# Optimization experiments

Measured on AMD Instinct MI355X. Metric: run time of the kernel, lower is better.

The kernel has to match this reference:

```python
import jax, jax.numpy as jnp
import numpy as np

NUM_GRAPHS = 1024
NODES_PER_GRAPH = 128
NUM_EDGES = 1048576
D_IN = 128          # n_heads * head_out_feats = input/concat dim
ATT_HEADS = 2       # intra/inter GATConv(d, 32, 2) as in HDN-DDI repo
ATT_OUT = 32
POOL_HEADS = 2      # pool = GATConv(128, 64, 2)
POOL_OUT = 64
EPS = 1e-5          # PyG LayerNorm eps


def _segment_softmax(e, seg, n):
    # numerically-stable softmax over edges grouped by destination node
    m = jax.ops.segment_max(e, seg, num_segments=n)
    m = jnp.where(jnp.isfinite(m), m, 0.0)
    p = jnp.exp(e - m[seg])
    s = jax.ops.segment_sum(p, seg, num_segments=n)
    return p / (s[seg] + 1e-16)


def _gat(x_src, x_dst, edge_index, w_src, w_dst, att_src, att_dst, bias, self_loops):
    # PyG GATConv: linear -> per-head attention logits -> leaky_relu(0.2) ->
    # softmax over incoming edges -> weighted sum of source features -> concat heads + bias
    H, C = att_src.shape
    nd = x_dst.shape[0]
    hs = (x_src @ w_src).reshape(-1, H, C)   # [Ns,H,C]
    hd = (x_dst @ w_dst).reshape(-1, H, C)   # [Nd,H,C]
    a_s = jnp.einsum('nhc,hc->nh', hs, att_src)
    a_d = jnp.einsum('nhc,hc->nh', hd, att_dst)
    src, dst = edge_index[0], edge_index[1]
    if self_loops:  # PyG default add_self_loops=True (non-bipartite case)
        loop = jnp.arange(nd)
        src = jnp.concatenate([src, loop])
        dst = jnp.concatenate([dst, loop])
    e = jax.nn.leaky_relu(a_s[src] + a_d[dst], 0.2)  # [E,H]
    alpha = _segment_softmax(e, dst, nd)
    out = jax.ops.segment_sum(hs[src] * alpha[:, :, None], dst, num_segments=nd)
    return out.reshape(nd, H * C) + bias


def _graph_layernorm(x, batch, weight, bias, n_graphs):
    # PyG LayerNorm(mode='graph'): normalize over all nodes+channels of each graph
    f = x.shape[-1]
    cnt = jax.ops.segment_sum(jnp.ones((x.shape[0],), x.dtype), batch, num_segments=n_graphs)
    norm = jnp.maximum(cnt, 1.0) * f
    mean = jax.ops.segment_sum(x.sum(-1), batch, num_segments=n_graphs) / norm
    xc = x - mean[batch][:, None]
    var = jax.ops.segment_sum((xc * xc).sum(-1), batch, num_segments=n_graphs) / norm
    return (xc / jnp.sqrt(var + EPS)[batch][:, None]) * weight + bias


def setup_inputs() -> dict:
    key = jax.random.key(0)
    ks = jax.random.split(key, 24)
    B, P, E, D = NUM_GRAPHS, NODES_PER_GRAPH, NUM_EDGES, D_IN
    N = B * P

    def intra_edges(k):  # within-graph edges, no self-loops
        k1, k2, k3 = jax.random.split(k, 3)
        g = jax.random.randint(k1, (E,), 0, B)
        s = jax.random.randint(k2, (E,), 0, P)
        d = (s + 1 + jax.random.randint(k3, (E,), 0, P - 1)) % P
        return jnp.stack([g * P + s, g * P + d])

    def inter_edges(k):  # bipartite head-node -> tail-node edges within same graph pair
        k1, k2, k3 = jax.random.split(k, 3)
        g = jax.random.randint(k1, (E,), 0, B)
        s = jax.random.randint(k2, (E,), 0, P)
        d = jax.random.randint(k3, (E,), 0, P)
        return jnp.stack([g * P + s, g * P + d])

    batch = jnp.repeat(jnp.arange(B), P)
    # one global supernode (type 2) per graph: the last node
    y = jnp.tile(jnp.concatenate([jnp.zeros((P - 1,), jnp.int32), jnp.array([2], jnp.int32)]), B)
    p = lambda k, shape: jax.random.normal(k, shape, jnp.float32) * 0.1
    return {
        'h_x': jax.random.normal(ks[0], (N, D), jnp.float32),
        't_x': jax.random.normal(ks[1], (N, D), jnp.float32),
        'h_edge_index': intra_edges(ks[2]),
        't_edge_index': intra_edges(ks[3]),
        'b_edge_index': inter_edges(ks[4]),
        'h_batch': batch,
        't_batch': batch,
        'h_y': y,
        't_y': y,
        'w_intra': p(ks[5], (D, ATT_HEADS * ATT_OUT)),
        'att_intra_src': p(ks[6], (ATT_HEADS, ATT_OUT)),
        'att_intra_dst': p(ks[7], (ATT_HEADS, ATT_OUT)),
        'b_intra': jnp.zeros((ATT_HEADS * ATT_OUT,), jnp.float32),
        'w_inter_src': p(ks[8], (D, ATT_HEADS * ATT_OUT)),
        'w_inter_dst': p(ks[9], (D, ATT_HEADS * ATT_OUT)),
        'att_inter_src': p(ks[10], (ATT_HEADS, ATT_OUT)),
        'att_inter_dst': p(ks[11], (ATT_HEADS, ATT_OUT)),
        'b_inter': jnp.zeros((ATT_HEADS * ATT_OUT,), jnp.float32),
        'w_pool': p(ks[12], (D, POOL_HEADS * POOL_OUT)),
        'att_pool_src': p(ks[13], (POOL_HEADS, POOL_OUT)),
        'att_pool_dst': p(ks[14], (POOL_HEADS, POOL_OUT)),
        'b_pool': jnp.zeros((POOL_HEADS * POOL_OUT,), jnp.float32),
        'ln_weight': jnp.ones((D,), jnp.float32),
        'ln_bias': jnp.zeros((D,), jnp.float32),
    }


def reference(h_x, t_x, h_edge_index, t_edge_index, b_edge_index, h_batch, t_batch, h_y, t_y,
              w_intra, att_intra_src, att_intra_dst, b_intra,
              w_inter_src, w_inter_dst, att_inter_src, att_inter_dst, b_inter,
              w_pool, att_pool_src, att_pool_dst, b_pool, ln_weight, ln_bias):
    h_in = jax.nn.elu(h_x)
    t_in = jax.nn.elu(t_x)
    # intra-graph attention (shared GATConv applied to both drug graphs)
    h_intra = _gat(h_in, h_in, h_edge_index, w_intra, w_intra, att_intra_src, att_intra_dst, b_intra, True)
    t_intra = _gat(t_in, t_in, t_edge_index, w_intra, w_intra, att_intra_src, att_intra_dst, b_intra, True)
    # inter-graph (bipartite) attention: h->t and reversed t->h with shared weights
    t_inter = _gat(h_in, t_in, b_edge_index, w_inter_src, w_inter_dst, att_inter_src, att_inter_dst, b_inter, False)
    h_inter = _gat(t_in, h_in, b_edge_index[::-1], w_inter_src, w_inter_dst, att_inter_src, att_inter_dst, b_inter, False)
    h_rep = jnp.concatenate([h_intra, h_inter], 1)  # [N, 128]
    t_rep = jnp.concatenate([t_intra, t_inter], 1)
    h_nx = jax.nn.elu(_graph_layernorm(h_rep, h_batch, ln_weight, ln_bias, NUM_GRAPHS))
    t_nx = jax.nn.elu(_graph_layernorm(t_rep, t_batch, ln_weight, ln_bias, NUM_GRAPHS))
    h_out = _gat(h_nx, h_nx, h_edge_index, w_pool, w_pool, att_pool_src, att_pool_dst, b_pool, True)
    t_out = _gat(t_nx, t_nx, t_edge_index, w_pool, w_pool, att_pool_src, att_pool_dst, b_pool, True)
    # get_node: gather the single type-2 supernode per graph (exactly NUM_GRAPHS of them)
    h_idx = jnp.where(h_y == 2, size=NUM_GRAPHS)[0]
    t_idx = jnp.where(t_y == 2, size=NUM_GRAPHS)[0]
    return h_out, t_out, h_out[h_idx], t_out[t_idx]
```

## Files before the change

### kernel.cpp

```cpp
#include <hip/hip_runtime.h>
#include <hip/hip_bf16.h>

#define NN 131072
#define NG 1024
#define NE 1048576
#define EB 16384
#define NB 64
#define EMAX 1536

typedef __hip_bfloat16 bf16;
typedef __attribute__((ext_vector_type(8))) short short8v;
typedef __attribute__((ext_vector_type(4))) float f32x4;

__device__ __forceinline__ float b2f(bf16 v){ return __bfloat162float(v); }
__device__ __forceinline__ bf16 f2b(float v){ return __float2bfloat16(v); }
__device__ __forceinline__ unsigned short f2bu(float v){ bf16 b = f2b(v); return *(unsigned short*)&b; }
__device__ __forceinline__ float eluf(float x){ return x > 0.f ? x : expm1f(x); }
__device__ __forceinline__ float lrelu(float x){ return x >= 0.f ? x : 0.2f*x; }

__device__ __forceinline__ float ldx(const void* p, size_t i, int f){
  return f ? ((const float*)p)[i] : b2f(((const bf16*)p)[i]);
}

struct EPtrs { const int *s0,*d0,*s1,*d1,*s2,*d2,*s3,*d3; };

__global__ void detect_dtype(const unsigned short* __restrict__ x, int* __restrict__ flag){
  if (blockIdx.x==0 && threadIdx.x==0){
    int bad = 0;
    for (int i=0;i<2048;i++){
      unsigned short e = (x[i] >> 7) & 0xFF;
      if (e == 0xFF) bad++;
      else if (e >= 0x90) bad++;
      else if (e != 0 && e < 0x60) bad++;
    }
    *flag = (bad > 64) ? 1 : 0;
  }
}

__global__ __launch_bounds__(256) void hist_bagg(EPtrs ep, int* __restrict__ Hb){
  __shared__ int cnt[NG];
  int set = blockIdx.y, blk = blockIdx.x, t = threadIdx.x;
  const int* dp = set==0 ? ep.d0 : set==1 ? ep.d1 : set==2 ? ep.d2 : ep.d3;
  for (int i=t;i<NG;i+=256) cnt[i]=0;
  __syncthreads();
  int e0 = blk*EB;
  for (int i=t;i<EB;i+=256) atomicAdd(&cnt[dp[e0+i]>>7],1);
  __syncthreads();
  for (int i=t;i<NG;i+=256) Hb[((size_t)set*NB+blk)*NG+i] = cnt[i];
}

__global__ __launch_bounds__(1024) void scan_bagg(const int* __restrict__ Hb, int* __restrict__ Bb,
                                                  int* __restrict__ base_gs){
  __shared__ int sh[1024];
  int set = blockIdx.x, t = threadIdx.x;
  int run = 0;
  for (int b=0;b<NB;b++){
    int v = Hb[((size_t)set*NB + b)*NG + t];
    Bb[((size_t)set*NB + b)*NG + t] = run;
    run += v;
  }
  int val = run; sh[t] = run; __syncthreads();
  for (int d=1; d<1024; d<<=1){
    int add = (t>=d)? sh[t-d] : 0; __syncthreads();
    val += add; sh[t] = val; __syncthreads();
  }
  int binbase = val - run;
  base_gs[set*(NG+1) + t] = binbase;
  if (t==1023) base_gs[set*(NG+1)+NG] = val;
  for (int b=0;b<NB;b++) Bb[((size_t)set*NB + b)*NG + t] += binbase;
}

__global__ __launch_bounds__(256) void scatter_bagg(EPtrs ep, const int* __restrict__ Bb,
                                                    unsigned short* __restrict__ pk){
  __shared__ int cur[NG];
  int set = blockIdx.y, blk = blockIdx.x, t = threadIdx.x;
  const int* sp = set==0 ? ep.s0 : set==1 ? ep.s1 : set==2 ? ep.s2 : ep.s3;
  const int* dp = set==0 ? ep.d0 : set==1 ? ep.d1 : set==2 ? ep.d2 : ep.d3;
  for (int i=t;i<NG;i+=256) cur[i] = Bb[((size_t)set*NB+blk)*NG+i];
  __syncthreads();
  int e0 = blk*EB;
  for (int i=t;i<EB;i+=256){
    int e = e0+i;
    int d = dp[e], s = sp[e];
    int p = atomicAdd(&cur[d>>7],1);
    pk[(size_t)set*NE + p] = (unsigned short)(((d & 127) << 8) | (s & 127));
  }
}

__global__ __launch_bounds__(256) void build_csr(const unsigned short* __restrict__ pk, const int* __restrict__ base,
                                                 unsigned char* __restrict__ srcs8, int* __restrict__ offs4){
  __shared__ int hist[128], excl[128], cur[128];
  __shared__ unsigned char ob[8192];
  int set = blockIdx.y, g = blockIdx.x, t = threadIdx.x;
  int n0 = base[set*(NG+1) + g], n1 = base[set*(NG+1) + g + 1];
  int cnt = min(n1 - n0, 8192);
  if (t < 128) hist[t] = 0;
  __syncthreads();
  const unsigned short* PK = pk + (size_t)set*NE + n0;
  for (int i=t; i<cnt; i+=256) atomicAdd(&hist[PK[i]>>8], 1);
  __syncthreads();
  if (t < 128) excl[t] = hist[t];
  __syncthreads();
  for (int d=1; d<128; d<<=1){
    int v = (t < 128 && t >= d) ? excl[t-d] : 0;
    __syncthreads();
    if (t < 128) excl[t] += v;
    __syncthreads();
  }
  if (t < 128){
    int e_ = excl[t] - hist[t];
    cur[t] = e_;
    offs4[(size_t)set*(NN+1) + g*128 + t] = n0 + e_;
  }
  if (g == NG-1 && t == 0) offs4[(size_t)set*(NN+1) + NN] = NE;
  __syncthreads();
  for (int i=t; i<cnt; i+=256){
    unsigned short v = PK[i];
    int p = atomicAdd(&cur[v>>8], 1);
    ob[p] = (unsigned char)(v & 127);
  }
  __syncthreads();
  unsigned char* S = srcs8 + (size_t)set*NE + n0;
  for (int i=t; i<cnt; i+=256) S[i] = ob[i];
}

__global__ __launch_bounds__(256) void prep_kernel(
    const void* w_intra, const void* w_isrc, const void* w_idst, const void* att_xd, const void* w_pool,
    const void* att_is, const void* att_id, const void* att_xs,
    const void* att_ps, const void* att_pd,
    const void* b_intra, const void* b_inter, const void* b_pool,
    const void* ln_w, const void* ln_b,
    bf16* __restrict__ Wtc, bf16* __restrict__ Wtp, float* __restrict__ vdst, float* __restrict__ sm,
    const int* __restrict__ fp){
  int f = *fp;
  int t = threadIdx.x;
  for (int i=t; i<16384; i+=256){
    int j = i & 7, l = (i>>3) & 63, ks = (i>>9) & 3, nt = i >> 11;
    int k = ks*32 + ((l>>4)<<3) + j;
    int c = nt*16 + (l & 15);
    float w1 = (c < 64) ? ldx(w_intra, k*64 + c, f) : ldx(w_isrc, k*64 + (c-64), f);
    Wtc[i] = f2b(w1);
    Wtp[i] = f2b(ldx(w_pool, k*128 + c, f));
  }
  {
    int k = t>>1, h = t&1; float a = 0.f;
    for (int c=0;c<32;c++) a += ldx(w_idst, k*64 + h*32 + c, f) * ldx(att_xd, h*32 + c, f);
    vdst[t] = a;
  }
  if (t < 64){
    sm[t]     = ldx(att_is, t, f);
    sm[64+t]  = ldx(att_id, t, f);
    sm[128+t] = ldx(att_xs, t, f);
    sm[448+t] = ldx(b_intra, t, f);
    sm[512+t] = ldx(b_inter, t, f);
  }
  if (t < 128){
    sm[192+t] = ldx(att_ps, t, f);
    sm[320+t] = ldx(att_pd, t, f);
    sm[576+t] = ldx(b_pool, t, f);
    sm[704+t] = ldx(ln_w, t, f);
    sm[832+t] = ldx(ln_b, t, f);
  }
}

__global__ __launch_bounds__(256) void avec_dx_m(const void* Xh, const void* Xt, const float* __restrict__ vdst,
                                                 float* __restrict__ aDx_h, float* __restrict__ aDx_t,
                                                 const int* __restrict__ fp){
  int f = *fp;
  int gid = blockIdx.x*256 + threadIdx.x;
  int n = gid >> 6, lane = gid & 63;
  int side = n >= NN;
  const void* X = side ? Xt : Xh;
  float* aDx = side ? aDx_t : aDx_h;
  int nl = side ? n - NN : n;
  float x1 = eluf(ldx(X, (size_t)nl*128 + lane, f));
  float x2 = eluf(ldx(X, (size_t)nl*128 + 64 + lane, f));
  float t0 = x1*vdst[lane*2+0] + x2*vdst[(lane+64)*2+0];
  float t1 = x1*vdst[lane*2+1] + x2*vdst[(lane+64)*2+1];
  #pragma unroll
  for (int o=32;o;o>>=1){ t0 += __shfl_xor(t0,o); t1 += __shfl_xor(t1,o); }
  if (lane == 0){ aDx[nl*2+0] = t0; aDx[nl*2+1] = t1; }
}

struct L1Set {
  const int* offs;
  const unsigned char* srcs;
  int a_side;
  int wt_half;
  int att_mode;
  int col_off;
  const float* aDx;
  bf16* repout;
};
struct L1Set4 { L1Set s[4]; };

__global__ __launch_bounds__(512) void gat_l1(L1Set4 sets, const void* Xh, const void* Xt,
    const bf16* __restrict__ Wtc, const float* __restrict__ sm, const int* __restrict__ fp){
  __shared__ char U[34816];
  __shared__ bf16 Ft[32*136];
  __shared__ float atab[192];
  __shared__ float2 aSl[128], aDl[128];
  __shared__ float rsum[128];
  __shared__ unsigned char ss[EMAX];
  __shared__ int begs[129];
  const L1Set S = sets.s[blockIdx.y];
  int g = blockIdx.x, t = threadIdx.x;
  int f = *fp;
  const void* A = S.a_side ? Xt : Xh;

  bf16* WtL = (bf16*)U;
  {
    const short8v* src = (const short8v*)(Wtc + (size_t)S.wt_half*8192);
    short8v* dst = (short8v*)WtL;
    #pragma unroll
    for (int i=0;i<2;i++) dst[t + i*512] = src[t + i*512];
  }
  if (t < 129) begs[t] = S.offs[g*128 + t];
  if (t < 192){
    float v;
    if (t < 64) v = sm[(S.att_mode ? 128 : 0) + t];
    else if (t < 128) v = sm[64 + (t-64)];
    else v = sm[(S.att_mode ? 512 : 448) + (t-128)];
    atab[t] = v;
  }
  __syncthreads();
  int gbeg = begs[0], Eg = min(begs[128]-gbeg, EMAX);
  for (int i=t; i<Eg; i+=512) ss[i] = S.srcs[gbeg + i];

  int w = t>>6, l = t&63, lr = l&15, lg = l>>4;
  size_t row = (size_t)g*128 + w*16 + lr;
  f32x4 acc[4];
  #pragma unroll
  for (int nt=0;nt<4;nt++) acc[nt] = (f32x4){0.f,0.f,0.f,0.f};
  #pragma unroll
  for (int ks=0;ks<4;ks++){
    short8v af;
    size_t ab = row*128 + ks*32 + lg*8;
    if (f){
      const float* Af = (const float*)A;
      #pragma unroll
      for (int j=0;j<8;j++){ ((unsigned short*)&af)[j] = f2bu(eluf(Af[ab+j])); }
    } else {
      const unsigned short* Au = (const unsigned short*)A;
      short8v raw = *(const short8v*)(Au + ab);
      #pragma unroll
      for (int j=0;j<8;j++){
        bf16 b; *(unsigned short*)&b = ((unsigned short*)&raw)[j];
        ((unsigned short*)&af)[j] = f2bu(eluf(b2f(b)));
      }
    }
    #pragma unroll
    for (int nt=0;nt<4;nt++){
      short8v bfr = *(const short8v*)((const unsigned short*)WtL + (size_t)((nt*4+ks)*64 + l)*8);
      acc[nt] = __builtin_amdgcn_mfma_f32_16x16x32_bf16(af, bfr, acc[nt], 0, 0, 0);
    }
  }
  #pragma unroll
  for (int rg=0; rg<4; ++rg){
    float pS0=0.f,pS1=0.f,pD0=0.f,pD1=0.f;
    #pragma unroll
    for (int nt=0;nt<4;nt++){
      float v = acc[nt][rg];
      int c = nt*16 + lr;
      float a = atab[c], b = atab[64+c];
      if (nt<2){ pS0 += v*a; pD0 += v*b; } else { pS1 += v*a; pD1 += v*b; }
    }
    #pragma unroll
    for (int o=1;o<16;o<<=1){
      pS0+=__shfl_xor(pS0,o); pS1+=__shfl_xor(pS1,o);
      pD0+=__shfl_xor(pD0,o); pD1+=__shfl_xor(pD1,o);
    }
    if (lr == 0){
      int rr = w*16 + lg*4 + rg;
      aSl[rr] = make_float2(pS0, pS1);
      if (S.att_mode == 0) aDl[rr] = make_float2(pD0, pD1);
    }
  }
  if (S.att_mode == 1 && t < 128) aDl[t] = ((const float2*)S.aDx)[g*128 + t];
  __syncthreads();

  bf16* Pm = (bf16*)U;
  #pragma unroll
  for (int h=0; h<2; ++h){
    for (int i=t; i<128*68; i+=512) ((unsigned int*)Pm)[i] = 0;
    #pragma unroll
    for (int ntl=0; ntl<2; ++ntl){
      int nt = h*2 + ntl;
      #pragma unroll
      for (int rg=0; rg<4; ++rg)
        ((unsigned short*)Ft)[(ntl*16+lr)*136 + (w*16+lg*4+rg)] = f2bu(acc[nt][rg]);
    }
    __syncthreads();
    if (t < 128){
      int r = t;
      float ad = h ? aDl[r].y : aDl[r].x;
      int b = begs[r]-gbeg, e = min(begs[r+1]-gbeg, EMAX);
      float rs = 0.f;
      unsigned short* Pr = (unsigned short*)Pm + r*136;
      for (int j=b; j<e; ++j){
        int s = ss[j];
        float as = h ? aSl[s].y : aSl[s].x;
        float p = __expf(lrelu(as + ad));
        bf16 ov; *(unsigned short*)&ov = Pr[s];
        Pr[s] = f2bu(b2f(ov) + p);
        rs += p;
      }
      if (S.att_mode == 0){
        float as = h ? aSl[r].y : aSl[r].x;
        float p = __expf(lrelu(as + ad));
        bf16 ov; *(unsigned short*)&ov = Pr[r];
        Pr[r] = f2bu(b2f(ov) + p);
        rs += p;
      }
      rsum[r] = rs;
    }
    __syncthreads();
    f32x4 a2[2];
    a2[0] = (f32x4){0.f,0.f,0.f,0.f}; a2[1] = (f32x4){0.f,0.f,0.f,0.f};
    #pragma unroll
    for (int ks=0;ks<4;ks++){
      short8v af = *(const short8v*)((const unsigned short*)Pm + (w*16+lr)*136 + ks*32 + lg*8);
      #pragma unroll
      for (int j=0;j<2;j++){
        short8v bfr = *(const short8v*)((const unsigned short*)Ft + (j*16+lr)*136 + ks*32 + lg*8);
        a2[j] = __builtin_amdgcn_mfma_f32_16x16x32_bf16(af, bfr, a2[j], 0, 0, 0);
      }
    }
    #pragma unroll
    for (int rg=0; rg<4; ++rg){
      int rrow = w*16 + lg*4 + rg;
      float rinv = 1.f / (rsum[rrow] + 1e-16f);
      size_t n = (size_t)g*128 + rrow;
      #pragma unroll
      for (int j=0;j<2;j++){
        int c = h*32 + j*16 + lr;
        float o = a2[j][rg]*rinv + atab[128+c];
        S.repout[n*128 + S.col_off + c] = f2b(o);
      }
    }
    __syncthreads();
  }
}

__global__ __launch_bounds__(512) void gat_pool(const bf16* __restrict__ rep,
    const int* __restrict__ offs_h, const unsigned char* __restrict__ srcs_h,
    const int* __restrict__ offs_t, const unsigned char* __restrict__ srcs_t,
    const bf16* __restrict__ Wtp, const float* __restrict__ sm,
    void* out, const int* __restrict__ fp){
  __shared__ char U[34816];
  __shared__ bf16 Ft[64*136];
  __shared__ float attL[384];
  __shared__ float2 aSp[128], aDp[128];
  __shared__ float rsum[128];
  __shared__ unsigned char ss[EMAX];
  __shared__ int begs[129];
  int side = blockIdx.y, g = blockIdx.x, t = threadIdx.x;
  int f = *fp;
  const int* offs = side ? offs_t : offs_h;
  const unsigned char* srcs = side ? srcs_t : srcs_h;
  const unsigned short* A = (const unsigned short*)rep + (size_t)side*NN*128;
  size_t obase = (size_t)side*NN*128;
  size_t gbase = (size_t)2*NN*128 + (size_t)side*NG*128;

  bf16* WtL = (bf16*)U;
  {
    const short8v* src = (const short8v*)Wtp;
    short8v* dst = (short8v*)WtL;
    #pragma unroll
    for (int i=0;i<4;i++) dst[t + i*512] = src[t + i*512];
  }
  if (t < 129) begs[t] = offs[g*128 + t];
  if (t < 384) attL[t] = sm[(t<128) ? 192+t : (t<256) ? 320+(t-128) : 576+(t-256)];
  __syncthreads();
  int gbeg = begs[0], Eg = min(begs[128]-gbeg, EMAX);
  for (int i=t; i<Eg; i+=512) ss[i] = srcs[gbeg + i];

  int w = t>>6, l = t&63, lr = l&15, lg = l>>4;
  size_t row = (size_t)g*128 + w*16 + lr;
  f32x4 acc[8];
  #pragma unroll
  for (int nt=0;nt<8;nt++) acc[nt] = (f32x4){0.f,0.f,0.f,0.f};
  #pragma unroll
  for (int ks=0;ks<4;ks++){
    short8v af = *(const short8v*)(A + row*128 + ks*32 + lg*8);
    #pragma unroll
    for (int nt=0;nt<8;nt++){
      short8v bfr = *(const short8v*)((const unsigned short*)WtL + (size_t)((nt*4+ks)*64 + l)*8);
      acc[nt] = __builtin_amdgcn_mfma_f32_16x16x32_bf16(af, bfr, acc[nt], 0, 0, 0);
    }
  }
  #pragma unroll
  for (int rg=0; rg<4; ++rg){
    float pS0=0.f,pS1=0.f,pD0=0.f,pD1=0.f;
    #pragma unroll
    for (int nt=0;nt<8;nt++){
      float v = acc[nt][rg];
      int c = nt*16 + lr;
      float a = attL[c], b = attL[128+c];
      if (nt<4){ pS0 += v*a; pD0 += v*b; } else { pS1 += v*a; pD1 += v*b; }
    }
    #pragma unroll
    for (int o=1;o<16;o<<=1){
      pS0+=__shfl_xor(pS0,o); pS1+=__shfl_xor(pS1,o);
      pD0+=__shfl_xor(pD0,o); pD1+=__shfl_xor(pD1,o);
    }
    if (lr == 0){
      int rr = w*16 + lg*4 + rg;
      aSp[rr] = make_float2(pS0, pS1);
      aDp[rr] = make_float2(pD0, pD1);
    }
  }
  __syncthreads();

  bf16* Pm = (bf16*)U;
  #pragma unroll
  for (int h=0; h<2; ++h){
    for (int i=t; i<128*68; i+=512) ((unsigned int*)Pm)[i] = 0;
    #pragma unroll
    for (int ntl=0; ntl<4; ++ntl){
      int nt = h*4 + ntl;
      #pragma unroll
      for (int rg=0; rg<4; ++rg)
        ((unsigned short*)Ft)[(ntl*16+lr)*136 + (w*16+lg*4+rg)] = f2bu(acc[nt][rg]);
    }
    __syncthreads();
    if (t < 128){
      int r = t;
      float ad = h ? aDp[r].y : aDp[r].x;
      int b = begs[r]-gbeg, e = min(begs[r+1]-gbeg, EMAX);
      float rs = 0.f;
      unsigned short* Pr = (unsigned short*)Pm + r*136;
      for (int j=b; j<e; ++j){
        int s = ss[j];
        float as = h ? aSp[s].y : aSp[s].x;
        float p = __expf(lrelu(as + ad));
        bf16 ov; *(unsigned short*)&ov = Pr[s];
        Pr[s] = f2bu(b2f(ov) + p);
        rs += p;
      }
      {
        float as = h ? aSp[r].y : aSp[r].x;
        float p = __expf(lrelu(as + ad));
        bf16 ov; *(unsigned short*)&ov = Pr[r];
        Pr[r] = f2bu(b2f(ov) + p);
        rs += p;
      }
      rsum[r] = rs;
    }
    __syncthreads();
    f32x4 a2[4];
    #pragma unroll
    for (int j=0;j<4;j++) a2[j] = (f32x4){0.f,0.f,0.f,0.f};
    #pragma unroll
    for (int ks=0;ks<4;ks++){
      short8v af = *(const short8v*)((const unsigned short*)Pm + (w*16+lr)*136 + ks*32 + lg*8);
      #pragma unroll
      for (int j=0;j<4;j++){
        short8v bfr = *(const short8v*)((const unsigned short*)Ft + (j*16+lr)*136 + ks*32 + lg*8);
        a2[j] = __builtin_amdgcn_mfma_f32_16x16x32_bf16(af, bfr, a2[j], 0, 0, 0);
      }
    }
    #pragma unroll
    for (int rg=0; rg<4; ++rg){
      int rrow = w*16 + lg*4 + rg;
      float rinv = 1.f / (rsum[rrow] + 1e-16f);
      size_t n = (size_t)g*128 + rrow;
      bool gw = (rrow == 127);
      #pragma unroll
      for (int j=0;j<4;j++){
        int c = h*64 + j*16 + lr;
        float o = a2[j][rg]*rinv + attL[256+c];
        size_t oi = obase + n*128 + c;
        if (f){
          ((float*)out)[oi] = o;
          if (gw) ((float*)out)[gbase + (size_t)g*128 + c] = o;
        } else {
          ((bf16*)out)[oi] = f2b(o);
          if (gw) ((bf16*)out)[gbase + (size_t)g*128 + c] = f2b(o);
        }
      }
    }
    __syncthreads();
  }
}

__global__ __launch_bounds__(512) void graph_ln_w(bf16* __restrict__ R_,
    const float* __restrict__ wv, const float* __restrict__ bv){
  __shared__ float sh1[8], sh2[8];
  int g = blockIdx.x, t = threadIdx.x;
  unsigned short* Ru = (unsigned short*)(R_ + (size_t)g*16384);
  short8v v[4];
  #pragma unroll
  for (int q=0;q<4;q++) v[q] = *(short8v*)(Ru + q*4096 + t*8);
  float s1=0.f, s2=0.f;
  #pragma unroll
  for (int q=0;q<4;q++)
    #pragma unroll
    for (int j=0;j<8;j++){
      bf16 b; *(unsigned short*)&b = ((unsigned short*)&v[q])[j];
      float x = b2f(b); s1 += x; s2 += x*x;
    }
  #pragma unroll
  for (int o=32;o;o>>=1){ s1 += __shfl_xor(s1,o); s2 += __shfl_xor(s2,o); }
  if ((t&63)==0){ sh1[t>>6]=s1; sh2[t>>6]=s2; }
  __syncthreads();
  float S1=0.f,S2=0.f;
  #pragma unroll
  for (int i=0;i<8;i++){ S1+=sh1[i]; S2+=sh2[i]; }
  float mean = S1 * (1.f/16384.f);
  float var = fmaxf(S2*(1.f/16384.f) - mean*mean, 0.f);
  float rstd = rsqrtf(var + 1e-5f);
  #pragma unroll
  for (int q=0;q<4;q++){
    short8v ov;
    #pragma unroll
    for (int j=0;j<8;j++){
      int c = (t*8 + j) & 127;
      bf16 b; *(unsigned short*)&b = ((unsigned short*)&v[q])[j];
      float y = (b2f(b)-mean)*rstd*wv[c] + bv[c];
      ((unsigned short*)&ov)[j] = f2bu(y>0.f ? y : expm1f(y));
    }
    *(short8v*)(Ru + q*4096 + t*8) = ov;
  }
}

extern "C" void kernel_launch(void* const* d_in, const int* in_sizes, int n_in,
                              void* d_out, int out_size, void* d_ws, size_t ws_size,
                              hipStream_t stream){
  (void)in_sizes; (void)n_in; (void)out_size; (void)ws_size;
  const void* h_x = d_in[0];
  const void* t_x = d_in[1];
  const int* h_ei = (const int*)d_in[2];
  const int* t_ei = (const int*)d_in[3];
  const int* b_ei = (const int*)d_in[4];

  char* base = (char*)d_ws;
  size_t off = 0;
  auto alloc = [&](size_t bytes)->char*{ char* p = base + off; off += (bytes + 255) & ~(size_t)255; return p; };
  bf16* rep      = (bf16*)alloc((size_t)2*NN*128*2);
  unsigned short* pk = (unsigned short*)alloc((size_t)4*NE*2);
  unsigned char* srcs8 = (unsigned char*)alloc((size_t)4*NE);
  int* offs4     = (int*)alloc((size_t)4*(NN+1)*4);
  int* Hb        = (int*)alloc((size_t)4*NB*NG*4);
  int* Bb        = (int*)alloc((size_t)4*NB*NG*4);
  int* base_gs   = (int*)alloc((size_t)4*(NG+1)*4);
  float* aDx_h   = (float*)alloc((size_t)NN*2*4);
  float* aDx_t   = (float*)alloc((size_t)NN*2*4);
  bf16* Wtc      = (bf16*)alloc(16384*2);
  bf16* Wtp      = (bf16*)alloc(16384*2);
  float* vdst    = (float*)alloc(256*4);
  float* sm      = (float*)alloc(960*4);
  int* flag      = (int*)alloc(256);

  bf16* rep_h = rep;
  bf16* rep_t = rep + (size_t)NN*128;

  detect_dtype<<<1,64,0,stream>>>((const unsigned short*)h_x, flag);

  EPtrs ep;
  ep.s0 = h_ei;      ep.d0 = h_ei + NE;
  ep.s1 = t_ei;      ep.d1 = t_ei + NE;
  ep.s2 = b_ei;      ep.d2 = b_ei + NE;
  ep.s3 = b_ei + NE; ep.d3 = b_ei;
  hist_bagg<<<dim3(NB,4),256,0,stream>>>(ep, Hb);
  scan_bagg<<<4,1024,0,stream>>>(Hb, Bb, base_gs);
  scatter_bagg<<<dim3(NB,4),256,0,stream>>>(ep, Bb, pk);
  build_csr<<<dim3(NG,4),256,0,stream>>>(pk, base_gs, srcs8, offs4);

  prep_kernel<<<1,256,0,stream>>>(d_in[9], d_in[13], d_in[14], d_in[16], d_in[18],
      d_in[10], d_in[11], d_in[15], d_in[19], d_in[20],
      d_in[12], d_in[17], d_in[21], d_in[22], d_in[23],
      Wtc, Wtp, vdst, sm, flag);

  avec_dx_m<<<65536,256,0,stream>>>(h_x, t_x, vdst, aDx_h, aDx_t, flag);

  const int* offs_h = offs4;
  const int* offs_t = offs4 + (NN+1);
  const int* offs_ht= offs4 + 2*(NN+1);
  const int* offs_th= offs4 + 3*(NN+1);
  const unsigned char* srcs_h = srcs8;
  const unsigned char* srcs_t = srcs8 + NE;
  const unsigned char* srcs_ht= srcs8 + (size_t)2*NE;
  const unsigned char* srcs_th= srcs8 + (size_t)3*NE;

  {
    L1Set4 L;
    L.s[0] = { offs_h,  srcs_h,  0, 0, 0, 0,  nullptr, rep_h };
    L.s[1] = { offs_t,  srcs_t,  1, 0, 0, 0,  nullptr, rep_t };
    L.s[2] = { offs_ht, srcs_ht, 0, 1, 1, 64, aDx_t,   rep_t };
    L.s[3] = { offs_th, srcs_th, 1, 1, 1, 64, aDx_h,   rep_h };
    gat_l1<<<dim3(NG,4),512,0,stream>>>(L, h_x, t_x, Wtc, sm, flag);
  }

  graph_ln_w<<<2048,512,0,stream>>>(rep, sm+704, sm+832);

  gat_pool<<<dim3(NG,2),512,0,stream>>>(rep, offs_h, srcs_h, offs_t, srcs_t,
      Wtp, sm, d_out, flag);
}
```

Before: 585.4 us.

## Merge layer-1 GAT sets per side and split pool GAT into GEMM plus aggregation

The layer-1 kernel now runs one block per graph side and computes the intra and inter projections in a single 128-wide GEMM, so each input tile is loaded and ELU-transformed once instead of twice. It then runs both aggregation passes, writing the inter result into the other side's representation. The pool layer is split into a standalone GEMM that overwrites rep in place with projected features and global attention logits, followed by a templated aggregation kernel. This aims to reduce redundant input reads and per-block register and LDS pressure, at the cost of an extra global round trip for the projected features and logits.

```diff
diff --git a/kernel.cpp b/kernel.cpp
--- a/kernel.cpp
+++ b/kernel.cpp
@@ -182,56 +182,48 @@
   if (lane == 0){ aDx[nl*2+0] = t0; aDx[nl*2+1] = t1; }
 }
 
-struct L1Set {
-  const int* offs;
-  const unsigned char* srcs;
-  int a_side;
-  int wt_half;
-  int att_mode;
-  int col_off;
-  const float* aDx;
-  bf16* repout;
-};
-struct L1Set4 { L1Set s[4]; };
-
-__global__ __launch_bounds__(512) void gat_l1(L1Set4 sets, const void* Xh, const void* Xt,
-    const bf16* __restrict__ Wtc, const float* __restrict__ sm, const int* __restrict__ fp){
+__global__ __launch_bounds__(512) void gat_l1v2(
+    const void* Xh, const void* Xt,
+    const int* __restrict__ offs_h, const unsigned char* __restrict__ srcs_h,
+    const int* __restrict__ offs_t, const unsigned char* __restrict__ srcs_t,
+    const int* __restrict__ offs_ht, const unsigned char* __restrict__ srcs_ht,
+    const int* __restrict__ offs_th, const unsigned char* __restrict__ srcs_th,
+    const float* __restrict__ aDx_h, const float* __restrict__ aDx_t,
+    bf16* __restrict__ rep, const bf16* __restrict__ Wtc,
+    const float* __restrict__ sm, const int* __restrict__ fp){
   __shared__ char U[34816];
   __shared__ bf16 Ft[32*136];
-  __shared__ float atab[192];
-  __shared__ float2 aSl[128], aDl[128];
+  __shared__ float atab[320];
+  __shared__ float2 aSi[128], aDi[128], aSx[128];
   __shared__ float rsum[128];
-  __shared__ unsigned char ss[EMAX];
-  __shared__ int begs[129];
-  const L1Set S = sets.s[blockIdx.y];
-  int g = blockIdx.x, t = threadIdx.x;
+  __shared__ int begs_i[129], begs_x[129];
+  int side = blockIdx.y, g = blockIdx.x, t = threadIdx.x;
   int f = *fp;
-  const void* A = S.a_side ? Xt : Xh;
+  const void* A = side ? Xt : Xh;
+  const int* offs_int = side ? offs_t : offs_h;
+  const unsigned char* srcs_int = side ? srcs_t : srcs_h;
+  const int* offs_ext = side ? offs_th : offs_ht;
+  const unsigned char* srcs_ext = side ? srcs_th : srcs_ht;
+  const float* aDxo = side ? aDx_h : aDx_t;
+  bf16* rep_self  = rep + (size_t)side*NN*128;
+  bf16* rep_other = rep + (size_t)(1-side)*NN*128;
 
   bf16* WtL = (bf16*)U;
   {
-    const short8v* src = (const short8v*)(Wtc + (size_t)S.wt_half*8192);
+    const short8v* src = (const short8v*)Wtc;
     short8v* dst = (short8v*)WtL;
     #pragma unroll
-    for (int i=0;i<2;i++) dst[t + i*512] = src[t + i*512];
-  }
-  if (t < 129) begs[t] = S.offs[g*128 + t];
-  if (t < 192){
-    float v;
-    if (t < 64) v = sm[(S.att_mode ? 128 : 0) + t];
-    else if (t < 128) v = sm[64 + (t-64)];
-    else v = sm[(S.att_mode ? 512 : 448) + (t-128)];
-    atab[t] = v;
-  }
-  __syncthreads();
-  int gbeg = begs[0], Eg = min(begs[128]-gbeg, EMAX);
-  for (int i=t; i<Eg; i+=512) ss[i] = S.srcs[gbeg + i];
+    for (int i=0;i<4;i++) dst[t + i*512] = src[t + i*512];
+  }
+  if (t < 129){ begs_i[t] = offs_int[g*128 + t]; begs_x[t] = offs_ext[g*128 + t]; }
+  if (t < 320) atab[t] = sm[ (t<192) ? t : (t<256 ? 448+(t-192) : 512+(t-256)) ];
+  __syncthreads();
 
   int w = t>>6, l = t&63, lr = l&15, lg = l>>4;
   size_t row = (size_t)g*128 + w*16 + lr;
-  f32x4 acc[4];
-  #pragma unroll
-  for (int nt=0;nt<4;nt++) acc[nt] = (f32x4){0.f,0.f,0.f,0.f};
+  f32x4 acc[8];
+  #pragma unroll
+  for (int nt=0;nt<8;nt++) acc[nt] = (f32x4){0.f,0.f,0.f,0.f};
   #pragma unroll
   for (int ks=0;ks<4;ks++){
     short8v af;
@@ -239,7 +231,7 @@
     if (f){
       const float* Af = (const float*)A;
       #pragma unroll
-      for (int j=0;j<8;j++){ ((unsigned short*)&af)[j] = f2bu(eluf(Af[ab+j])); }
+      for (int j=0;j<8;j++) ((unsigned short*)&af)[j] = f2bu(eluf(Af[ab+j]));
     } else {
       const unsigned short* Au = (const unsigned short*)A;
       short8v raw = *(const short8v*)(Au + ab);
@@ -250,237 +242,111 @@
       }
     }
     #pragma unroll
-    for (int nt=0;nt<4;nt++){
+    for (int nt=0;nt<8;nt++){
       short8v bfr = *(const short8v*)((const unsigned short*)WtL + (size_t)((nt*4+ks)*64 + l)*8);
       acc[nt] = __builtin_amdgcn_mfma_f32_16x16x32_bf16(af, bfr, acc[nt], 0, 0, 0);
     }
   }
   #pragma unroll
   for (int rg=0; rg<4; ++rg){
-    float pS0=0.f,pS1=0.f,pD0=0.f,pD1=0.f;
-    #pragma unroll
-    for (int nt=0;nt<4;nt++){
+    float pS0=0.f,pS1=0.f,pD0=0.f,pD1=0.f,pX0=0.f,pX1=0.f;
+    #pragma unroll
+    for (int nt=0;nt<8;nt++){
       float v = acc[nt][rg];
       int c = nt*16 + lr;
-      float a = atab[c], b = atab[64+c];
-      if (nt<2){ pS0 += v*a; pD0 += v*b; } else { pS1 += v*a; pD1 += v*b; }
+      if (nt<4){
+        float a=atab[c], b=atab[64+c];
+        if (nt<2){ pS0+=v*a; pD0+=v*b; } else { pS1+=v*a; pD1+=v*b; }
+      } else {
+        float xw=atab[128+(c-64)];
+        if (nt<6) pX0+=v*xw; else pX1+=v*xw;
+      }
     }
     #pragma unroll
     for (int o=1;o<16;o<<=1){
       pS0+=__shfl_xor(pS0,o); pS1+=__shfl_xor(pS1,o);
       pD0+=__shfl_xor(pD0,o); pD1+=__shfl_xor(pD1,o);
+      pX0+=__shfl_xor(pX0,o); pX1+=__shfl_xor(pX1,o);
     }
     if (lr == 0){
       int rr = w*16 + lg*4 + rg;
-      aSl[rr] = make_float2(pS0, pS1);
-      if (S.att_mode == 0) aDl[rr] = make_float2(pD0, pD1);
-    }
-  }
-  if (S.att_mode == 1 && t < 128) aDl[t] = ((const float2*)S.aDx)[g*128 + t];
+      aSi[rr] = make_float2(pS0, pS1);
+      aDi[rr] = make_float2(pD0, pD1);
+      aSx[rr] = make_float2(pX0, pX1);
+    }
+  }
   __syncthreads();
 
   bf16* Pm = (bf16*)U;
-  #pragma unroll
-  for (int h=0; h<2; ++h){
-    for (int i=t; i<128*68; i+=512) ((unsigned int*)Pm)[i] = 0;
-    #pragma unroll
-    for (int ntl=0; ntl<2; ++ntl){
-      int nt = h*2 + ntl;
+  for (int sx=0; sx<2; ++sx){
+    const int* begs = sx ? begs_x : begs_i;
+    const unsigned char* srcs = sx ? srcs_ext : srcs_int;
+    int gbeg = begs[0];
+    bf16* repout = sx ? rep_other : rep_self;
+    int col_base = sx ? 64 : 0;
+    #pragma unroll
+    for (int h=0; h<2; ++h){
+      for (int i=t; i<128*68; i+=512) ((unsigned int*)Pm)[i] = 0;
       #pragma unroll
-      for (int rg=0; rg<4; ++rg)
-        ((unsigned short*)Ft)[(ntl*16+lr)*136 + (w*16+lg*4+rg)] = f2bu(acc[nt][rg]);
-    }
-    __syncthreads();
-    if (t < 128){
-      int r = t;
-      float ad = h ? aDl[r].y : aDl[r].x;
-      int b = begs[r]-gbeg, e = min(begs[r+1]-gbeg, EMAX);
-      float rs = 0.f;
-      unsigned short* Pr = (unsigned short*)Pm + r*136;
-      for (int j=b; j<e; ++j){
-        int s = ss[j];
-        float as = h ? aSl[s].y : aSl[s].x;
-        float p = __expf(lrelu(as + ad));
-        bf16 ov; *(unsigned short*)&ov = Pr[s];
-        Pr[s] = f2bu(b2f(ov) + p);
-        rs += p;
-      }
-      if (S.att_mode == 0){
-        float as = h ? aSl[r].y : aSl[r].x;
-        float p = __expf(lrelu(as + ad));
-        bf16 ov; *(unsigned short*)&ov = Pr[r];
-        Pr[r] = f2bu(b2f(ov) + p);
-        rs += p;
-      }
-      rsum[r] = rs;
-    }
-    __syncthreads();
-    f32x4 a2[2];
-    a2[0] = (f32x4){0.f,0.f,0.f,0.f}; a2[1] = (f32x4){0.f,0.f,0.f,0.f};
-    #pragma unroll
-    for (int ks=0;ks<4;ks++){
-      short8v af = *(const short8v*)((const unsigned short*)Pm + (w*16+lr)*136 + ks*32 + lg*8);
+      for (int ntl=0; ntl<2; ++ntl){
+        int nt = sx*4 + h*2 + ntl;
+        #pragma unroll
+        for (int rg=0; rg<4; ++rg)
+          ((unsigned short*)Ft)[(ntl*16+lr)*136 + (w*16+lg*4+rg)] = f2bu(acc[nt][rg]);
+      }
+      __syncthreads();
+      if (t < 128){
+        int r = t;
+        float ad;
+        if (sx){ float2 d = ((const float2*)aDxo)[g*128+r]; ad = h ? d.y : d.x; }
+        else   { ad = h ? aDi[r].y : aDi[r].x; }
+        int b = begs[r]-gbeg, e = begs[r+1]-gbeg;
+        float rs = 0.f;
+        unsigned short* Pr = (unsigned short*)Pm + r*136;
+        const float2* aSt = sx ? aSx : aSi;
+        for (int j=b; j<e; ++j){
+          int s = srcs[gbeg + j];
+          float as = h ? aSt[s].y : aSt[s].x;
+          float p = __expf(lrelu(as + ad));
+          bf16 ov; *(unsigned short*)&ov = Pr[s];
+          Pr[s] = f2bu(b2f(ov) + p);
+          rs += p;
+        }
+        if (sx == 0){
+          float as = h ? aSt[r].y : aSt[r].x;
+          float p = __expf(lrelu(as + ad));
+          bf16 ov; *(unsigned short*)&ov = Pr[r];
+          Pr[r] = f2bu(b2f(ov) + p);
+          rs += p;
+        }
+        rsum[r] = rs;
+      }
+      __syncthreads();
+      f32x4 a2[2];
+      a2[0] = (f32x4){0.f,0.f,0.f,0.f}; a2[1] = (f32x4){0.f,0.f,0.f,0.f};
       #pragma unroll
-      for (int j=0;j<2;j++){
-        short8v bfr = *(const short8v*)((const unsigned short*)Ft + (j*16+lr)*136 + ks*32 + lg*8);
-        a2[j] = __builtin_amdgcn_mfma_f32_16x16x32_bf16(af, bfr, a2[j], 0, 0, 0);
-      }
-    }
-    #pragma unroll
-    for (int rg=0; rg<4; ++rg){
-      int rrow = w*16 + lg*4 + rg;
-      float rinv = 1.f / (rsum[rrow] + 1e-16f);
-      size_t n = (size_t)g*128 + rrow;
+      for (int ks=0;ks<4;ks++){
+        short8v af = *(const short8v*)((const unsigned short*)Pm + (w*16+lr)*136 + ks*32 + lg*8);
+        #pragma unroll
+        for (int j=0;j<2;j++){
+          short8v bfr = *(const short8v*)((const unsigned short*)Ft + (j*16+lr)*136 + ks*32 + lg*8);
+          a2[j] = __builtin_amdgcn_mfma_f32_16x16x32_bf16(af, bfr, a2[j], 0, 0, 0);
+        }
+      }
       #pragma unroll
-      for (int j=0;j<2;j++){
-        int c = h*32 + j*16 + lr;
-        float o = a2[j][rg]*rinv + atab[128+c];
-        S.repout[n*128 + S.col_off + c] = f2b(o);
-      }
-    }
-    __syncthreads();
-  }
-}
-
-__global__ __launch_bounds__(512) void gat_pool(const bf16* __restrict__ rep,
-    const int* __restrict__ offs_h, const unsigned char* __restrict__ srcs_h,
-    const int* __restrict__ offs_t, const unsigned char* __restrict__ srcs_t,
-    const bf16* __restrict__ Wtp, const float* __restrict__ sm,
-    void* out, const int* __restrict__ fp){
-  __shared__ char U[34816];
-  __shared__ bf16 Ft[64*136];
-  __shared__ float attL[384];
-  __shared__ float2 aSp[128], aDp[128];
-  __shared__ float rsum[128];
-  __shared__ unsigned char ss[EMAX];
-  __shared__ int begs[129];
-  int side = blockIdx.y, g = blockIdx.x, t = threadIdx.x;
-  int f = *fp;
-  const int* offs = side ? offs_t : offs_h;
-  const unsigned char* srcs = side ? srcs_t : srcs_h;
-  const unsigned short* A = (const unsigned short*)rep + (size_t)side*NN*128;
-  size_t obase = (size_t)side*NN*128;
-  size_t gbase = (size_t)2*NN*128 + (size_t)side*NG*128;
-
-  bf16* WtL = (bf16*)U;
-  {
-    const short8v* src = (const short8v*)Wtp;
-    short8v* dst = (short8v*)WtL;
-    #pragma unroll
-    for (int i=0;i<4;i++) dst[t + i*512] = src[t + i*512];
-  }
-  if (t < 129) begs[t] = offs[g*128 + t];
-  if (t < 384) attL[t] = sm[(t<128) ? 192+t : (t<256) ? 320+(t-128) : 576+(t-256)];
-  __syncthreads();
-  int gbeg = begs[0], Eg = min(begs[128]-gbeg, EMAX);
-  for (int i=t; i<Eg; i+=512) ss[i] = srcs[gbeg + i];
-
-  int w = t>>6, l = t&63, lr = l&15, lg = l>>4;
-  size_t row = (size_t)g*128 + w*16 + lr;
-  f32x4 acc[8];
-  #pragma unroll
-  for (int nt=0;nt<8;nt++) acc[nt] = (f32x4){0.f,0.f,0.f,0.f};
-  #pragma unroll
-  for (int ks=0;ks<4;ks++){
-    short8v af = *(const short8v*)(A + row*128 + ks*32 + lg*8);
-    #pragma unroll
-    for (int nt=0;nt<8;nt++){
-      short8v bfr = *(const short8v*)((const unsigned short*)WtL + (size_t)((nt*4+ks)*64 + l)*8);
-      acc[nt] = __builtin_amdgcn_mfma_f32_16x16x32_bf16(af, bfr, acc[nt], 0, 0, 0);
-    }
-  }
-  #pragma unroll
-  for (int rg=0; rg<4; ++rg){
-    float pS0=0.f,pS1=0.f,pD0=0.f,pD1=0.f;
-    #pragma unroll
-    for (int nt=0;nt<8;nt++){
-      float v = acc[nt][rg];
-      int c = nt*16 + lr;
-      float a = attL[c], b = attL[128+c];
-      if (nt<4){ pS0 += v*a; pD0 += v*b; } else { pS1 += v*a; pD1 += v*b; }
-    }
-    #pragma unroll
-    for (int o=1;o<16;o<<=1){
-      pS0+=__shfl_xor(pS0,o); pS1+=__shfl_xor(pS1,o);
-      pD0+=__shfl_xor(pD0,o); pD1+=__shfl_xor(pD1,o);
-    }
-    if (lr == 0){
-      int rr = w*16 + lg*4 + rg;
-      aSp[rr] = make_float2(pS0, pS1);
-      aDp[rr] = make_float2(pD0, pD1);
-    }
-  }
-  __syncthreads();
-
-  bf16* Pm = (bf16*)U;
-  #pragma unroll
-  for (int h=0; h<2; ++h){
-    for (int i=t; i<128*68; i+=512) ((unsigned int*)Pm)[i] = 0;
-    #pragma unroll
-    for (int ntl=0; ntl<4; ++ntl){
-      int nt = h*4 + ntl;
-      #pragma unroll
-      for (int rg=0; rg<4; ++rg)
-        ((unsigned short*)Ft)[(ntl*16+lr)*136 + (w*16+lg*4+rg)] = f2bu(acc[nt][rg]);
-    }
-    __syncthreads();
-    if (t < 128){
-      int r = t;
-      float ad = h ? aDp[r].y : aDp[r].x;
-      int b = begs[r]-gbeg, e = min(begs[r+1]-gbeg, EMAX);
-      float rs = 0.f;
-      unsigned short* Pr = (unsigned short*)Pm + r*136;
-      for (int j=b; j<e; ++j){
-        int s = ss[j];
-        float as = h ? aSp[s].y : aSp[s].x;
-        float p = __expf(lrelu(as + ad));
-        bf16 ov; *(unsigned short*)&ov = Pr[s];
-        Pr[s] = f2bu(b2f(ov) + p);
-        rs += p;
-      }
-      {
-        float as = h ? aSp[r].y : aSp[r].x;
-        float p = __expf(lrelu(as + ad));
-        bf16 ov; *(unsigned short*)&ov = Pr[r];
-        Pr[r] = f2bu(b2f(ov) + p);
-        rs += p;
-      }
-      rsum[r] = rs;
-    }
-    __syncthreads();
-    f32x4 a2[4];
-    #pragma unroll
-    for (int j=0;j<4;j++) a2[j] = (f32x4){0.f,0.f,0.f,0.f};
-    #pragma unroll
-    for (int ks=0;ks<4;ks++){
-      short8v af = *(const short8v*)((const unsigned short*)Pm + (w*16+lr)*136 + ks*32 + lg*8);
-      #pragma unroll
-      for (int j=0;j<4;j++){
-        short8v bfr = *(const short8v*)((const unsigned short*)Ft + (j*16+lr)*136 + ks*32 + lg*8);
-        a2[j] = __builtin_amdgcn_mfma_f32_16x16x32_bf16(af, bfr, a2[j], 0, 0, 0);
-      }
-    }
-    #pragma unroll
-    for (int rg=0; rg<4; ++rg){
-      int rrow = w*16 + lg*4 + rg;
-      float rinv = 1.f / (rsum[rrow] + 1e-16f);
-      size_t n = (size_t)g*128 + rrow;
-      bool gw = (rrow == 127);
-      #pragma unroll
-      for (int j=0;j<4;j++){
-        int c = h*64 + j*16 + lr;
-        float o = a2[j][rg]*rinv + attL[256+c];
-        size_t oi = obase + n*128 + c;
-        if (f){
-          ((float*)out)[oi] = o;
-          if (gw) ((float*)out)[gbase + (size_t)g*128 + c] = o;
-        } else {
-          ((bf16*)out)[oi] = f2b(o);
-          if (gw) ((bf16*)out)[gbase + (size_t)g*128 + c] = f2b(o);
+      for (int rg=0; rg<4; ++rg){
+        int rrow = w*16 + lg*4 + rg;
+        float rinv = 1.f / (rsum[rrow] + 1e-16f);
+        size_t n = (size_t)g*128 + rrow;
+        #pragma unroll
+        for (int j=0;j<2;j++){
+          int c = h*32 + j*16 + lr;
+          float o = a2[j][rg]*rinv + atab[(sx?256:192) + c];
+          repout[n*128 + col_base + c] = f2b(o);
         }
       }
-    }
-    __syncthreads();
+      __syncthreads();
+    }
   }
 }
 
@@ -521,6 +387,182 @@
       ((unsigned short*)&ov)[j] = f2bu(y>0.f ? y : expm1f(y));
     }
     *(short8v*)(Ru + q*4096 + t*8) = ov;
+  }
+}
+
+__global__ __launch_bounds__(512) void gemm_pool(bf16* __restrict__ rep, const bf16* __restrict__ Wtp,
+    const float* __restrict__ sm,
+    float* __restrict__ aSp_h, float* __restrict__ aDp_h,
+    float* __restrict__ aSp_t, float* __restrict__ aDp_t){
+  __shared__ bf16 WtL[16384];
+  __shared__ float attL[256];
+  int side = blockIdx.x >> 10;
+  int bx = blockIdx.x & 1023;
+  unsigned short* A = (unsigned short*)rep + (size_t)side*NN*128;
+  float* oS = side ? aSp_t : aSp_h;
+  float* oD = side ? aDp_t : aDp_h;
+  int tid = threadIdx.x;
+  {
+    const short8v* src = (const short8v*)Wtp;
+    short8v* dst = (short8v*)WtL;
+    #pragma unroll
+    for (int i=0;i<4;i++) dst[tid + i*512] = src[tid + i*512];
+    if (tid < 256) attL[tid] = sm[(tid<128) ? 192+tid : 320+(tid-128)];
+  }
+  __syncthreads();
+  int w = tid >> 6, l = tid & 63;
+  int lr = l & 15, lg = l >> 4;
+  size_t row = (size_t)bx*128 + w*16 + lr;
+  f32x4 acc[8];
+  #pragma unroll
+  for (int nt=0;nt<8;nt++) acc[nt] = (f32x4){0.f,0.f,0.f,0.f};
+  #pragma unroll
+  for (int ks=0;ks<4;ks++){
+    short8v af = *(const short8v*)(A + row*128 + ks*32 + lg*8);
+    #pragma unroll
+    for (int nt=0;nt<8;nt++){
+      short8v bfr = *(const short8v*)((const unsigned short*)WtL + (size_t)((nt*4+ks)*64 + l)*8);
+      acc[nt] = __builtin_amdgcn_mfma_f32_16x16x32_bf16(af, bfr, acc[nt], 0, 0, 0);
+    }
+  }
+  size_t crow = (size_t)bx*128 + w*16 + lg*4;
+  #pragma unroll
+  for (int nt=0;nt<8;nt++)
+    #pragma unroll
+    for (int r=0;r<4;r++)
+      ((bf16*)A)[(crow + r)*128 + nt*16 + lr] = f2b(acc[nt][r]);
+  #pragma unroll
+  for (int rg=0; rg<4; ++rg){
+    float pS0=0.f,pS1=0.f,pD0=0.f,pD1=0.f;
+    #pragma unroll
+    for (int nt=0;nt<8;nt++){
+      float v = acc[nt][rg];
+      int c = nt*16 + lr;
+      float a=attL[c], b=attL[128+c];
+      if (nt<4){ pS0+=v*a; pD0+=v*b; } else { pS1+=v*a; pD1+=v*b; }
+    }
+    #pragma unroll
+    for (int o=1;o<16;o<<=1){
+      pS0+=__shfl_xor(pS0,o); pS1+=__shfl_xor(pS1,o);
+      pD0+=__shfl_xor(pD0,o); pD1+=__shfl_xor(pD1,o);
+    }
+    if (lr == 0){
+      size_t n = crow + rg;
+      oS[n*2]=pS0; oS[n*2+1]=pS1;
+      oD[n*2]=pD0; oD[n*2+1]=pD1;
+    }
+  }
+}
+
+struct GatSet {
+  const int* offs;
+  const unsigned char* srcs;
+  const bf16* F;
+  const float* aS;
+  const float* aD;
+  const float* bias;
+  int col_in;
+  int self_loops;
+  int col_off;
+  int pad;
+  size_t obase_bf, obase_f32, gbase;
+};
+struct GatSet4 { GatSet s[4]; };
+
+template<int FD>
+__global__ __launch_bounds__(512) void gat_mfma(GatSet4 sets, void* out,
+    const int* __restrict__ fp, const int* __restrict__ fsel){
+  constexpr int NH = FD/2;
+  constexpr int NT = NH/16;
+  constexpr int KSH = (FD==64)?5:6;
+  __shared__ bf16 Ft[NH*136];
+  __shared__ bf16 Pm[128*136];
+  __shared__ float2 aSs[128];
+  __shared__ float rsum[128];
+  __shared__ unsigned char ss[EMAX];
+  __shared__ int begs[129];
+  const GatSet S = sets.s[blockIdx.y];
+  int fo = fp ? *fp : -1;
+  size_t obase = (fsel && *fsel) ? S.obase_f32 : S.obase_bf;
+  int g = blockIdx.x, t = threadIdx.x;
+
+  if (t < 129) begs[t] = S.offs[g*128 + t];
+  if (t >= 256 && t < 384) aSs[t-256] = ((const float2*)S.aS)[g*128 + (t-256)];
+  __syncthreads();
+  int gbeg = begs[0];
+  int Eg = min(begs[128] - gbeg, EMAX);
+  int w = t >> 6, l = t & 63, lr = l & 15, lg = l >> 4;
+
+  #pragma unroll
+  for (int h=0; h<2; ++h){
+    for (int i=t; i<128*68; i+=512) ((unsigned int*)Pm)[i] = 0;
+    if (h==0) for (int i=t; i<Eg; i+=512) ss[i] = S.srcs[gbeg + i];
+    __syncthreads();
+    if (t < 128){
+      int r = t;
+      float ad = S.aD[(size_t)(g*128+r)*2 + h];
+      int b = begs[r]-gbeg, e = min(begs[r+1]-gbeg, EMAX);
+      float rs = 0.f;
+      unsigned short* Pr = (unsigned short*)Pm + r*136;
+      for (int j=b; j<e; ++j){
+        int s = ss[j];
+        float2 as2 = aSs[s];
+        float p = __expf(lrelu((h ? as2.y : as2.x) + ad));
+        bf16 ov; *(unsigned short*)&ov = Pr[s];
+        Pr[s] = f2bu(b2f(ov) + p);
+        rs += p;
+      }
+      if (S.self_loops){
+        float2 as2 = aSs[r];
+        float p = __expf(lrelu((h ? as2.y : as2.x) + ad));
+        bf16 ov; *(unsigned short*)&ov = Pr[r];
+        Pr[r] = f2bu(b2f(ov) + p);
+        rs += p;
+      }
+      rsum[r] = rs;
+    } else {
+      const unsigned short* Fu = (const unsigned short*)S.F;
+      unsigned short* FtU = (unsigned short*)Ft;
+      int ft = t - 128;
+      for (int i=ft; i<NH*128; i+=384){
+        int c = i & (NH-1), k = i >> KSH;
+        FtU[c*136 + k] = Fu[((size_t)(g*128+k))*128 + S.col_in + h*NH + c];
+      }
+    }
+    __syncthreads();
+    f32x4 acc[NT];
+    #pragma unroll
+    for (int nt=0;nt<NT;nt++) acc[nt] = (f32x4){0.f,0.f,0.f,0.f};
+    #pragma unroll
+    for (int ks=0;ks<4;ks++){
+      short8v af = *(const short8v*)((const unsigned short*)Pm + (w*16+lr)*136 + ks*32 + lg*8);
+      #pragma unroll
+      for (int nt=0;nt<NT;nt++){
+        short8v bfr = *(const short8v*)((const unsigned short*)Ft + (nt*16 + lr)*136 + ks*32 + lg*8);
+        acc[nt] = __builtin_amdgcn_mfma_f32_16x16x32_bf16(af, bfr, acc[nt], 0, 0, 0);
+      }
+    }
+    #pragma unroll
+    for (int rg=0; rg<4; ++rg){
+      int rrow = w*16 + lg*4 + rg;
+      float rinv = 1.f / (rsum[rrow] + 1e-16f);
+      int n = g*128 + rrow;
+      bool gw = (fp != nullptr) && (rrow == 127);
+      #pragma unroll
+      for (int nt=0;nt<NT;nt++){
+        int c = h*NH + nt*16 + lr;
+        float o = acc[nt][rg]*rinv + S.bias[c];
+        size_t oi = obase + (size_t)n*128 + S.col_off + c;
+        if (fo > 0){
+          ((float*)out)[oi] = o;
+          if (gw) ((float*)out)[S.gbase + (size_t)g*128 + c] = o;
+        } else {
+          ((bf16*)out)[oi] = f2b(o);
+          if (gw) ((bf16*)out)[S.gbase + (size_t)g*128 + c] = f2b(o);
+        }
+      }
+    }
+    __syncthreads();
   }
 }
 
@@ -546,6 +588,10 @@
   int* base_gs   = (int*)alloc((size_t)4*(NG+1)*4);
   float* aDx_h   = (float*)alloc((size_t)NN*2*4);
   float* aDx_t   = (float*)alloc((size_t)NN*2*4);
+  float* aSp_h   = (float*)alloc((size_t)NN*2*4);
+  float* aDp_h   = (float*)alloc((size_t)NN*2*4);
+  float* aSp_t   = (float*)alloc((size_t)NN*2*4);
+  float* aDp_t   = (float*)alloc((size_t)NN*2*4);
   bf16* Wtc      = (bf16*)alloc(16384*2);
   bf16* Wtp      = (bf16*)alloc(16384*2);
   float* vdst    = (float*)alloc(256*4);
@@ -583,17 +629,21 @@
   const unsigned char* srcs_ht= srcs8 + (size_t)2*NE;
   const unsigned char* srcs_th= srcs8 + (size_t)3*NE;
 
+  gat_l1v2<<<dim3(NG,2),512,0,stream>>>(h_x, t_x,
+      offs_h, srcs_h, offs_t, srcs_t, offs_ht, srcs_ht, offs_th, srcs_th,
+      aDx_h, aDx_t, rep, Wtc, sm, flag);
+
+  graph_ln_w<<<2048,512,0,stream>>>(rep, sm+704, sm+832);
+
+  gemm_pool<<<2048,512,0,stream>>>(rep, Wtp, sm, aSp_h, aDp_h, aSp_t, aDp_t);
+
   {
-    L1Set4 L;
-    L.s[0] = { offs_h,  srcs_h,  0, 0, 0, 0,  nullptr, rep_h };
-    L.s[1] = { offs_t,  srcs_t,  1, 0, 0, 0,  nullptr, rep_t };
-    L.s[2] = { offs_ht, srcs_ht, 0, 1, 1, 64, aDx_t,   rep_t };
-    L.s[3] = { offs_th, srcs_th, 1, 1, 1, 64, aDx_h,   rep_h };
-    gat_l1<<<dim3(NG,4),512,0,stream>>>(L, h_x, t_x, Wtc, sm, flag);
-  }
-
-  graph_ln_w<<<2048,512,0,stream>>>(rep, sm+704, sm+832);
-
-  gat_pool<<<dim3(NG,2),512,0,stream>>>(rep, offs_h, srcs_h, offs_t, srcs_t,
-      Wtp, sm, d_out, flag);
-}
+    size_t gb_h = (size_t)2*NN*128;
+    size_t gb_t = gb_h + (size_t)NG*128;
+    GatSet4 P;
+    P.s[0] = { offs_h, srcs_h, rep_h, aSp_h, aDp_h, sm+576, 0, 1, 0, 0, 0,              0,              gb_h };
+    P.s[1] = { offs_t, srcs_t, rep_t, aSp_t, aDp_t, sm+576, 0, 1, 0, 0, (size_t)NN*128, (size_t)NN*128, gb_t };
+    P.s[2] = P.s[0]; P.s[3] = P.s[0];
+    gat_mfma<128><<<dim3(NG,2),512,0,stream>>>(P, d_out, flag, flag);
+  }
+}
```

Result: slower. 601.1 us (+2.7%).
